# Optimization experiments

Hardware: AMD Instinct MI355X
Metric: run time of the kernel (lower is better)

Reference implementation:

```python
import jax, jax.numpy as jnp
import numpy as np


def _box_iou(a, b):
    # a: [K,4], b: [K,4] in ltrb; returns [K,K] pairwise IoU (torchvision box_iou math)
    area_a = jnp.clip(a[:, 2] - a[:, 0], 0) * jnp.clip(a[:, 3] - a[:, 1], 0)
    area_b = jnp.clip(b[:, 2] - b[:, 0], 0) * jnp.clip(b[:, 3] - b[:, 1], 0)
    lt = jnp.maximum(a[:, None, :2], b[None, :, :2])
    rb = jnp.minimum(a[:, None, 2:], b[None, :, 2:])
    wh = jnp.clip(rb - lt, 0)
    inter = wh[..., 0] * wh[..., 1]
    return inter / (area_a[:, None] + area_b[None, :] - inter + 1e-9)


def _nms_class(score, boxes, th_c, nms_th, K):
    # score: [N], boxes: [N,4]. Keep boxes with score > th_c, take top-K by score,
    # then greedy NMS suppressing lower-scored boxes with IoU >= nms_th (original keeps iou < nms_th).
    masked = jnp.where(score > th_c, score, -jnp.inf)
    top_s, idx = jax.lax.top_k(masked, K)          # descending score order
    valid = top_s > -jnp.inf
    bk = boxes[idx]                                 # [K,4]
    iou = _box_iou(bk, bk)                          # [K,K]
    order = jnp.arange(K)

    def body(alive, i):
        keep_i = alive[i]
        suppress = keep_i & (iou[i] >= nms_th) & (order > i)
        return alive & ~suppress, keep_i

    _, keep = jax.lax.scan(body, valid, order)
    return jnp.where(keep[:, None], bk, 0.0), jnp.where(keep, top_s, 0.0), keep


def decode(bboxes_in, scores_in, dboxes_xywh, conf_th, nms_th, max_num, scale_xy, scale_wh):
    B, C = bboxes_in.shape[0], scores_in.shape[1]
    K = int(max_num)
    # scale_back_batch: xywh offsets -> ltrb absolute boxes, softmax over classes
    b = jnp.transpose(bboxes_in, (0, 2, 1))                         # [B,N,4]
    xy = scale_xy * b[..., :2] * dboxes_xywh[..., 2:] + dboxes_xywh[..., :2]
    wh = jnp.exp(scale_wh * b[..., 2:]) * dboxes_xywh[..., 2:]
    ltrb = jnp.concatenate([xy - 0.5 * wh, xy + 0.5 * wh], axis=-1)  # [B,N,4]
    probs = jax.nn.softmax(jnp.transpose(scores_in, (0, 2, 1)), axis=-1)  # [B,N,C]
    cls_scores = jnp.transpose(probs[..., 1:], (0, 2, 1))            # [B,C-1,N] (skip background cls 0)

    def per_image(scores_cn, boxes_n4):
        f = jax.vmap(lambda s, t: _nms_class(s, boxes_n4, t, nms_th, K))
        return f(scores_cn, conf_th)

    bk, sk, keep = jax.vmap(per_image)(cls_scores, ltrb)  # [B,C-1,K,4], [B,C-1,K], [B,C-1,K]
    M = (C - 1) * K
    labels = jnp.arange(1, C, dtype=jnp.float32)[None, :, None] * keep.astype(jnp.float32)
    return (bk.reshape(B, M, 4), labels.reshape(B, M), sk.reshape(B, M), keep.reshape(B, M))


def setup_inputs() -> dict:
    key = jax.random.key(0)
    k0, k1, k2, k3, k4 = jax.random.split(key, 5)
    B, N, C = 32, 24564, 21
    bboxes_in = 0.5 * jax.random.normal(k0, (B, 4, N), jnp.float32)
    scores_in = jax.random.normal(k1, (B, C, N), jnp.float32)
    cxy = jax.random.uniform(k2, (1, N, 2), jnp.float32)
    dwh = jax.random.uniform(k3, (1, N, 2), jnp.float32, 0.05, 0.5)
    dboxes_xywh = jnp.concatenate([cxy, dwh], axis=-1)
    conf_th = jax.random.uniform(k4, (C - 1,), jnp.float32, 0.01, 0.05)
    return {
        'bboxes_in': bboxes_in,
        'scores_in': scores_in,
        'dboxes_xywh': dboxes_xywh,
        'conf_th': conf_th,
        'nms_th': jnp.float32(0.5),
        'max_num': 200,
        'scale_xy': 0.1,
        'scale_wh': 0.2,
    }


def reference(bboxes_in, scores_in, dboxes_xywh, conf_th, nms_th, max_num, scale_xy, scale_wh):
    # Padded, jit-compatible equivalent of the torch Decoder: per image we return
    # [(C-1)*K] slots of (boxes, labels, scores) with a boolean keep-mask; the torch
    # version returns only the kept (variable-length) entries, in the same order.
    return decode(bboxes_in, scores_in, dboxes_xywh, conf_th, nms_th, max_num, scale_xy, scale_wh)
```

## Files before the change

kernel.cpp:

```cpp
#include <hip/hip_runtime.h>
#include <math.h>

typedef unsigned int uint;
typedef unsigned short u16;
typedef unsigned long long u64;

#define NT 256
#define KTOP 200
#define CAP 256
#define CAPC 3072
#define SEGS 4
#define SEGCAP 512
#define NCLS 21
#define C1 20
#define MROWS 208
#define NSPLIT 48

struct Rec { float4 box; double lse; double pad; };

__device__ __forceinline__ u64 flip64(double d) {
  u64 u = (u64)__double_as_longlong(d);
  return (u & 0x8000000000000000ULL) ? ~u : (u | 0x8000000000000000ULL);
}

__device__ __forceinline__ double unflip64(u64 k) {
  u64 u = (k & 0x8000000000000000ULL) ? (k ^ 0x8000000000000000ULL) : ~k;
  return __longlong_as_double((long long)u);
}

__device__ __forceinline__ uint q_key16(float sf) {
  float qf = (sf + 16.0f) * 4096.0f;
  qf = fmaxf(fminf(qf, 65535.0f), 1.0f);
  return (uint)qf;
}

__device__ __forceinline__ void par_walk(const uint* hist, uint* scan, u64* wm,
                                         uint* res, uint rank, int tid) {
  scan[tid] = hist[tid];
  __syncthreads();
#pragma unroll
  for (int off = 1; off < 256; off <<= 1) {
    uint v = scan[tid];
    uint a = (tid + off < 256) ? scan[tid + off] : 0u;
    __syncthreads();
    scan[tid] = v + a;
    __syncthreads();
  }
  u64 m = __ballot(scan[tid] >= rank);
  if ((tid & 63) == 0) wm[tid >> 6] = m;
  __syncthreads();
  if (tid == 0) {
    int bin = 0;
    for (int w = 3; w >= 0; --w) {
      if (wm[w]) { bin = w * 64 + (63 - __clzll(wm[w])); break; }
    }
    res[0] = (uint)bin;
    res[1] = scan[bin];
    res[2] = hist[bin];
  }
  __syncthreads();
}

__global__ __launch_bounds__(NT) void zero_ghist(uint* __restrict__ g) {
  g[(size_t)blockIdx.x * NT + threadIdx.x] = 0;
}

__global__ __launch_bounds__(NT) void prep_kernel(
    const float* __restrict__ bboxes, const float* __restrict__ scores,
    const float* __restrict__ dboxes, const float* __restrict__ conf_th,
    const float* __restrict__ scale_xy_p, const float* __restrict__ scale_wh_p,
    Rec* __restrict__ recs, u16* __restrict__ keys_out,
    uint* __restrict__ ghist,
    int B, int N, int npad, int perblk)
{
  __shared__ double s_logth[C1];
  __shared__ uint lhist[C1 * 256];
  int tid = threadIdx.x;
  if (tid < C1) s_logth[tid] = log((double)conf_th[tid]);
  for (int i = tid; i < C1 * 256; i += NT) lhist[i] = 0;
  __syncthreads();

  int b = blockIdx.x / NSPLIT, j = blockIdx.x - b * NSPLIT;
  int s0 = j * perblk, e0 = min(N, s0 + perblk);
  int half = (e0 - s0) >> 1;
  float sxy = *scale_xy_p, swh = *scale_wh_p;

  for (int p = tid; p < half; p += NT) {
    int n = s0 + 2 * p;
    const float* bb = bboxes + (size_t)b * 4 * N + n;
    float2 bx = *reinterpret_cast<const float2*>(bb);
    float2 by = *reinterpret_cast<const float2*>(bb + (size_t)N);
    float2 bw = *reinterpret_cast<const float2*>(bb + 2 * (size_t)N);
    float2 bh = *reinterpret_cast<const float2*>(bb + 3 * (size_t)N);
    float4 d0 = reinterpret_cast<const float4*>(dboxes)[n];
    float4 d1 = reinterpret_cast<const float4*>(dboxes)[n + 1];
    float x0 = sxy * bx.x * d0.z + d0.x;
    float y0 = sxy * by.x * d0.w + d0.y;
    float w0 = expf(swh * bw.x) * d0.z;
    float h0 = expf(swh * bh.x) * d0.w;
    float x1 = sxy * bx.y * d1.z + d1.x;
    float y1 = sxy * by.y * d1.w + d1.y;
    float w1 = expf(swh * bw.y) * d1.z;
    float h1 = expf(swh * bh.y) * d1.w;

    const float* sc = scores + (size_t)b * NCLS * N + n;
    float2 v[NCLS];
    float mx0 = -INFINITY, mx1 = -INFINITY;
#pragma unroll
    for (int c = 0; c < NCLS; ++c) {
      float2 t = *reinterpret_cast<const float2*>(sc + (size_t)c * N);
      v[c] = t;
      mx0 = fmaxf(mx0, t.x);
      mx1 = fmaxf(mx1, t.y);
    }
    double a0 = 0.0, a1 = 0.0, a2 = 0.0;
    double b0 = 0.0, b1 = 0.0, b2 = 0.0;
#pragma unroll
    for (int c = 0; c < NCLS; ++c) {
      float e0f = __expf(v[c].x - mx0);
      float e1f = __expf(v[c].y - mx1);
      if ((c % 3) == 0)      { a0 += (double)e0f; b0 += (double)e1f; }
      else if ((c % 3) == 1) { a1 += (double)e0f; b1 += (double)e1f; }
      else                   { a2 += (double)e0f; b2 += (double)e1f; }
    }
    double lse0 = (double)mx0 + log(a0 + a1 + a2);
    double lse1 = (double)mx1 + log(b0 + b1 + b2);

    int gid = b * N + n;
    Rec r0, r1;
    r0.box = make_float4(x0 - 0.5f * w0, y0 - 0.5f * h0, x0 + 0.5f * w0, y0 + 0.5f * h0);
    r0.lse = lse0; r0.pad = 0.0;
    r1.box = make_float4(x1 - 0.5f * w1, y1 - 0.5f * h1, x1 + 0.5f * w1, y1 + 0.5f * h1);
    r1.lse = lse1; r1.pad = 0.0;
    recs[gid] = r0;
    recs[gid + 1] = r1;

#pragma unroll
    for (int c = 0; c < C1; ++c) {
      double s0d = (double)v[c + 1].x - lse0;
      double s1d = (double)v[c + 1].y - lse1;
      uint k0 = 0, k1 = 0;
      if (s0d > s_logth[c]) k0 = q_key16((float)s0d);
      if (s1d > s_logth[c]) k1 = q_key16((float)s1d);
      *reinterpret_cast<uint*>(keys_out + ((size_t)b * C1 + c) * npad + n)
          = k0 | (k1 << 16);
      if (k0) atomicAdd(&lhist[c * 256 + (k0 >> 8)], 1u);
      if (k1) atomicAdd(&lhist[c * 256 + (k1 >> 8)], 1u);
    }
  }
  if (j == NSPLIT - 1 && npad > N) {
    int pad = npad - N;
    for (int t = tid; t < pad * C1; t += NT) {
      int c = t / pad, n = N + (t - c * pad);
      keys_out[((size_t)b * C1 + c) * npad + n] = 0;
    }
  }
  __syncthreads();
  for (int i = tid; i < C1 * 256; i += NT) {
    uint v2 = lhist[i];
    if (v2) atomicAdd(&ghist[((size_t)b * C1 + (i >> 8)) * 256 + (i & 255)], v2);
  }
}

__global__ __launch_bounds__(NT) void collect_kernel(
    const u16* __restrict__ keys, const uint* __restrict__ ghist,
    uint4* __restrict__ L0cnt, uint* __restrict__ cand, uint* __restrict__ cnts,
    int npad)
{
  int blk = blockIdx.x;
  int task = blk >> 2, seg = blk & (SEGS - 1);
  int tid = threadIdx.x, lane = tid & 63;
  __shared__ uint sL, sCnt0, sCnt;

  if (tid < 64) {
    uint4 h = reinterpret_cast<const uint4*>(ghist + (size_t)task * 256)[tid];
    uint s = h.x + h.y + h.z + h.w;
    uint suf = s;
#pragma unroll
    for (int off = 1; off < 64; off <<= 1) {
      uint o = (uint)__shfl_down((int)suf, off);
      if (lane + off < 64) suf += o;
    }
    uint total = (uint)__shfl((int)suf, 0);
    uint sn = (uint)__shfl_down((int)suf, 1);
    if (lane == 63) sn = 0;
    uint c3 = h.w + sn, c2 = c3 + h.z, c1 = c2 + h.y, c0 = c1 + h.x;
    uint binoff, cnt, abv;
    if (c3 >= KTOP)      { binoff = 3; cnt = c3; abv = c3 - h.w; }
    else if (c2 >= KTOP) { binoff = 2; cnt = c2; abv = c2 - h.z; }
    else if (c1 >= KTOP) { binoff = 1; cnt = c1; abv = c1 - h.y; }
    else                 { binoff = 0; cnt = c0; abv = c0 - h.x; }
    uint L0v, cnt0v, abovev;
    if (total < KTOP) {
      L0v = 1u; cnt0v = total; abovev = 0u;
    } else {
      u64 m = __ballot(suf >= KTOP);
      int l = 63 - __clzll(m);
      uint bo = (uint)__shfl((int)binoff, l);
      cnt0v = (uint)__shfl((int)cnt, l);
      abovev = (uint)__shfl((int)abv, l);
      L0v = ((uint)(4 * l) + bo) << 8;
    }
    if (lane == 0) {
      sL = L0v; sCnt0 = cnt0v;
      if (seg == 0) L0cnt[task] = make_uint4(L0v, cnt0v, abovev, total);
    }
  }
  if (tid == NT - 1) sCnt = 0;
  __syncthreads();

  uint L = sL, cnt0 = sCnt0;
  if (cnt0 > CAPC) { if (tid == 0) cnts[blk] = 0; return; }

  const u16* krow = keys + (size_t)task * npad;
  const uint4* krow8 = reinterpret_cast<const uint4*>(krow);
  int nv8 = npad >> 3;
  int per8 = (nv8 + SEGS - 1) >> 2;
  int s8 = seg * per8, e8 = min(nv8, s8 + per8);
  uint* myc = cand + ((size_t)task * SEGS + seg) * SEGCAP;

  for (int i = s8 + tid; i < e8; i += NT) {
    uint4 kv = krow8[i];
    uint base = (uint)(i << 3);
    uint ks[8] = { kv.x & 0xFFFFu, kv.x >> 16, kv.y & 0xFFFFu, kv.y >> 16,
                   kv.z & 0xFFFFu, kv.z >> 16, kv.w & 0xFFFFu, kv.w >> 16 };
#pragma unroll
    for (int comp = 0; comp < 8; ++comp) {
      uint k = ks[comp];
      bool f = (k >= L);
      u64 m = __ballot(f);
      if (m) {
        uint nb = (uint)__popcll(m);
        uint wb = 0;
        if (lane == 0) wb = atomicAdd(&sCnt, nb);
        wb = (uint)__shfl((int)wb, 0);
        if (f) {
          uint pos = wb + (uint)__popcll(m & ((1ULL << lane) - 1ULL));
          if (pos < SEGCAP) myc[pos] = (k << 15) | (base + comp);
        }
      }
    }
  }
  __syncthreads();
  if (tid == 0) cnts[blk] = sCnt;
}

__global__ __launch_bounds__(NT) void final_kernel(
    const u16* __restrict__ keys, const uint4* __restrict__ L0cnt,
    const uint* __restrict__ candg, const uint* __restrict__ cnts,
    const float* __restrict__ scores, const Rec* __restrict__ recs,
    const float* __restrict__ nms_th_p,
    float* __restrict__ out, int B, int N, int npad)
{
  int task = blockIdx.x;
  int b = task / C1, c = task - b * C1;
  int tid = threadIdx.x, lane = tid & 63, wav = tid >> 6;
  const u16* krow = keys + (size_t)task * npad;
  int nv8 = npad >> 3;

  __shared__ uint cand[CAPC];
  __shared__ uint histB[256];
  __shared__ uint scanB[256];
  __shared__ u64 wmB[4];
  __shared__ uint res3[4];
  __shared__ uint scq[SEGS];
  __shared__ int si[CAP];
  __shared__ u64 sC[CAP];
  __shared__ u64 skid[CAP];
  __shared__ float4 sbx[CAP];
  __shared__ float4 sbox[MROWS];
  __shared__ float sar[MROWS];
  __shared__ u64 smaskT[13][64];
  __shared__ u64 saliveW[4];
  __shared__ uint sCnt, sCnt2;

  uint4 w0 = L0cnt[task];
  uint cnt0 = w0.y;
  if (tid < SEGS) scq[tid] = cnts[task * SEGS + tid];
  if (tid == 0) { sCnt = 0; sCnt2 = 0; }
  if (tid < MROWS) { sbox[tid] = make_float4(0.f, 0.f, 0.f, 0.f); sar[tid] = 0.f; }
  __syncthreads();
  bool slow = (cnt0 > CAPC) ||
              (scq[0] > SEGCAP) || (scq[1] > SEGCAP) ||
              (scq[2] > SEGCAP) || (scq[3] > SEGCAP);

  uint pref = w0.x >> 8, above = w0.z, rank = KTOP - w0.z;
  uint cnt;

  if (!slow) {
    uint off1 = scq[0], off2 = off1 + scq[1], off3 = off2 + scq[2];
    cnt = off3 + scq[3];
    const uint* cg = candg + (size_t)task * SEGS * SEGCAP;
    for (int j = tid; j < (int)scq[0]; j += NT) cand[j] = cg[j];
    for (int j = tid; j < (int)scq[1]; j += NT) cand[off1 + j] = cg[SEGCAP + j];
    for (int j = tid; j < (int)scq[2]; j += NT) cand[off2 + j] = cg[2 * SEGCAP + j];
    for (int j = tid; j < (int)scq[3]; j += NT) cand[off3 + j] = cg[3 * SEGCAP + j];
    __syncthreads();
  } else {
    const uint4* krow8 = reinterpret_cast<const uint4*>(krow);
    histB[tid] = 0;
    __syncthreads();
    for (int i = tid; i < nv8; i += NT) {
      uint4 kv = krow8[i];
      uint ks[8] = { kv.x & 0xFFFFu, kv.x >> 16, kv.y & 0xFFFFu, kv.y >> 16,
                     kv.z & 0xFFFFu, kv.z >> 16, kv.w & 0xFFFFu, kv.w >> 16 };
#pragma unroll
      for (int comp = 0; comp < 8; ++comp) {
        uint k = ks[comp];
        if ((k >> 8) == pref) atomicAdd(&histB[k & 255u], 1u);
      }
    }
    __syncthreads();
    par_walk(histB, scanB, wmB, res3, rank, tid);
    uint Ts = (pref << 8) | res3[0];
    for (int i = tid; i < nv8; i += NT) {
      uint4 kv = krow8[i];
      uint base = (uint)(i << 3);
      uint ks[8] = { kv.x & 0xFFFFu, kv.x >> 16, kv.y & 0xFFFFu, kv.y >> 16,
                     kv.z & 0xFFFFu, kv.z >> 16, kv.w & 0xFFFFu, kv.w >> 16 };
#pragma unroll
      for (int comp = 0; comp < 8; ++comp) {
        uint k = ks[comp];
        bool f = (k >= Ts);
        u64 m = __ballot(f);
        if (m) {
          uint nb = (uint)__popcll(m);
          uint wb = 0;
          if (lane == 0) wb = atomicAdd(&sCnt, nb);
          wb = (uint)__shfl((int)wb, 0);
          if (f) {
            uint pos = wb + (uint)__popcll(m & ((1ULL << lane) - 1ULL));
            if (pos < CAPC) cand[pos] = (k << 15) | (base + comp);
          }
        }
      }
    }
    __syncthreads();
    cnt = min(sCnt, (uint)CAPC);
  }

  uint cntF;
  if (cnt <= CAP) {
    for (int p = tid; p < (int)cnt; p += NT) si[p] = (int)(cand[p] & 0x7FFFu);
    __syncthreads();
    cntF = cnt;
  } else {
    histB[tid] = 0;
    __syncthreads();
    for (int p = tid; p < (int)cnt; p += NT) {
      uint k = cand[p] >> 15;
      if ((k >> 8) == pref) atomicAdd(&histB[k & 255u], 1u);
    }
    __syncthreads();
    par_walk(histB, scanB, wmB, res3, rank, tid);
    uint T = (pref << 8) | res3[0];
    for (int p = tid; p < (int)cnt; p += NT) {
      uint cd = cand[p];
      if ((cd >> 15) >= T) {
        uint q = atomicAdd(&sCnt2, 1u);
        if (q < CAP) si[q] = (int)(cd & 0x7FFFu);
      }
    }
    __syncthreads();
    cntF = min(sCnt2, (uint)CAP);
  }

  int valid_cnt = (int)min(cntF, (uint)KTOP);

  {
    int p = tid;
    u64 C;
    if (p < (int)cntF) {
      int n = si[p];
      const Rec* rc = recs + (size_t)b * N + n;
      float4 box = rc->box;
      double l = rc->lse;
      double s = (double)scores[((size_t)b * NCLS + (c + 1)) * N + n] - l;
      u64 f = flip64(s);
      C = (f & ~0x7FFFULL) | (u64)(32767 - n);
      sbx[p] = box;
    } else {
      C = (u64)p;
      sbx[p] = make_float4(0.f, 0.f, 0.f, 0.f);
    }
    sC[p] = C;
  }
  __syncthreads();

  {
    u64 kp = sC[tid];
    int r = 0;
#pragma unroll 8
    for (int jj = 0; jj < CAP; ++jj) r += (sC[jj] > kp) ? 1 : 0;
    if (tid < (int)cntF && r < KTOP) {
      skid[r] = kp;
      float4 bx = sbx[tid];
      sbox[r] = bx;
      sar[r] = fmaxf(bx.z - bx.x, 0.f) * fmaxf(bx.w - bx.y, 0.f);
    }
  }
  __syncthreads();

  float nth = *nms_th_p;

  {
    float4 jb0 = sbox[lane], jb1 = sbox[lane + 64], jb2 = sbox[lane + 128];
    float4 jb3 = (lane + 192 < MROWS) ? sbox[lane + 192]
                                      : make_float4(0.f, 0.f, 0.f, 0.f);
    float ja0 = sar[lane], ja1 = sar[lane + 64], ja2 = sar[lane + 128],
          ja3 = (lane + 192 < MROWS) ? sar[lane + 192] : 0.f;
    for (int w = wav; w < 13; w += 4) {
      u64 word = 0;
      int r0 = w * 16;
#pragma unroll
      for (int rr = 0; rr < 16; ++rr) {
        int r = r0 + rr;
        float4 rb = sbox[r];
        float ra = sar[r];
        uint nib = 0;
#define IOU_BIT(K, JB, JA) { \
        int j = lane + 64 * (K); \
        float xx1 = fmaxf(rb.x, JB.x), yy1 = fmaxf(rb.y, JB.y); \
        float xx2 = fminf(rb.z, JB.z), yy2 = fminf(rb.w, JB.w); \
        float ww = fmaxf(xx2 - xx1, 0.f), hh = fmaxf(yy2 - yy1, 0.f); \
        float inter = ww * hh; \
        float den = ((ra + JA) - inter) + 1e-9f; \
        if ((inter >= nth * den) && (j > r)) nib |= 1u << (K); }
        IOU_BIT(0, jb0, ja0) IOU_BIT(1, jb1, ja1)
        IOU_BIT(2, jb2, ja2) IOU_BIT(3, jb3, ja3)
#undef IOU_BIT
        word |= (u64)nib << (rr * 4);
      }
      smaskT[w][lane] = word;
    }
  }
  __syncthreads();

  if (tid < 64) {
    u64 mm[13];
#pragma unroll
    for (int w = 0; w < 13; ++w) mm[w] = smaskT[w][lane];
    uint av = 0;
#pragma unroll
    for (int k = 0; k < 4; ++k)
      if (lane + 64 * k < valid_cnt) av |= 1u << k;
#define STEP(i) { \
    u64 bm = __ballot((lane == ((i) & 63)) && ((av >> ((i) >> 6)) & 1u)); \
    if (bm) av &= ~((uint)((mm[(i) >> 4] >> (((i) & 15) * 4)) & 0xFULL)); }
#define S4(i)  STEP(i) STEP((i)+1) STEP((i)+2) STEP((i)+3)
#define S16(i) S4(i) S4((i)+4) S4((i)+8) S4((i)+12)
#define S64(i) S16(i) S16((i)+16) S16((i)+32) S16((i)+48)
    S64(0) S64(64) S64(128) S16(192)
#undef S64
#undef S16
#undef S4
#undef STEP
#pragma unroll
    for (int k = 0; k < 4; ++k) {
      u64 bb2 = __ballot((av >> k) & 1u);
      if (lane == 0) saliveW[k] = bb2;
    }
  }
  __syncthreads();

  size_t M = (size_t)C1 * KTOP;
  float* out_boxes  = out;
  float* out_labels = out + (size_t)B * M * 4;
  float* out_scores = out_labels + (size_t)B * M;
  float* out_keep   = out_scores + (size_t)B * M;
  if (tid < KTOP) {
    size_t slot = ((size_t)b * C1 + c) * KTOP + tid;
    bool kept = (tid < valid_cnt) && ((saliveW[tid >> 6] >> (tid & 63)) & 1ULL);
    float4 bx = kept ? sbox[tid] : make_float4(0.f, 0.f, 0.f, 0.f);
    reinterpret_cast<float4*>(out_boxes)[slot] = bx;
    out_labels[slot] = kept ? (float)(c + 1) : 0.0f;
    out_scores[slot] = kept ? (float)exp(unflip64(skid[tid])) : 0.0f;
    out_keep[slot]   = kept ? 1.0f : 0.0f;
  }
}

extern "C" void kernel_launch(void* const* d_in, const int* in_sizes, int n_in,
                              void* d_out, int out_size, void* d_ws, size_t ws_size,
                              hipStream_t stream) {
  const float* bboxes   = (const float*)d_in[0];
  const float* scores   = (const float*)d_in[1];
  const float* dboxes   = (const float*)d_in[2];
  const float* conf_th  = (const float*)d_in[3];
  const float* nms_th   = (const float*)d_in[4];
  const float* scale_xy = (const float*)d_in[6];
  const float* scale_wh = (const float*)d_in[7];

  int N = in_sizes[2] / 4;
  int B = in_sizes[0] / (4 * N);
  int npad = (N + 7) & ~7;

  char* ws = (char*)d_ws;
  size_t off = 0;
  Rec*    recs    = (Rec*)   (ws + off); off += (size_t)B * N * sizeof(Rec);
  u16*    keys    = (u16*)   (ws + off); off += (size_t)B * C1 * npad * 2;
  uint*   ghist   = (uint*)  (ws + off); off += (size_t)B * C1 * 256 * 4;
  uint4*  L0cnt   = (uint4*) (ws + off); off += (size_t)B * C1 * 16;
  uint*   cand    = (uint*)  (ws + off); off += (size_t)B * C1 * SEGS * SEGCAP * 4;
  uint*   cnts    = (uint*)  (ws + off);

  zero_ghist<<<B * C1, NT, 0, stream>>>(ghist);

  int perblk = ((N + NSPLIT - 1) / NSPLIT + 1) & ~1;
  prep_kernel<<<B * NSPLIT, NT, 0, stream>>>(
      bboxes, scores, dboxes, conf_th, scale_xy, scale_wh,
      recs, keys, ghist, B, N, npad, perblk);

  collect_kernel<<<B * C1 * SEGS, NT, 0, stream>>>(
      keys, ghist, L0cnt, cand, cnts, npad);

  final_kernel<<<B * C1, NT, 0, stream>>>(
      keys, L0cnt, cand, cnts, scores, recs, nms_th,
      (float*)d_out, B, N, npad);
}
```

Before: 92.44 us.

## Split final kernel into top-k selection and NMS mask/resolve kernels

The final per-(image,class) kernel is divided into a top-k kernel, which writes the sorted top-200 keys and boxes to workspace, and a separate NMS kernel that builds the IoU bitmask and resolves survivors. Each kernel now needs less shared memory, so more blocks can be resident per CU. The cost is an extra launch and a global-memory round trip for the top-k keys and boxes.

```diff
diff --git a/kernel.cpp b/kernel.cpp
--- a/kernel.cpp
+++ b/kernel.cpp
@@ -245,16 +245,16 @@
   if (tid == 0) cnts[blk] = sCnt;
 }
 
-__global__ __launch_bounds__(NT) void final_kernel(
+__global__ __launch_bounds__(NT) void topk_kernel(
     const u16* __restrict__ keys, const uint4* __restrict__ L0cnt,
     const uint* __restrict__ candg, const uint* __restrict__ cnts,
     const float* __restrict__ scores, const Rec* __restrict__ recs,
-    const float* __restrict__ nms_th_p,
-    float* __restrict__ out, int B, int N, int npad)
+    u64* __restrict__ tkeys, float4* __restrict__ tbox, uint* __restrict__ tcnt,
+    int B, int N, int npad)
 {
   int task = blockIdx.x;
   int b = task / C1, c = task - b * C1;
-  int tid = threadIdx.x, lane = tid & 63, wav = tid >> 6;
+  int tid = threadIdx.x, lane = tid & 63;
   const u16* krow = keys + (size_t)task * npad;
   int nv8 = npad >> 3;
 
@@ -266,19 +266,13 @@
   __shared__ uint scq[SEGS];
   __shared__ int si[CAP];
   __shared__ u64 sC[CAP];
-  __shared__ u64 skid[CAP];
   __shared__ float4 sbx[CAP];
-  __shared__ float4 sbox[MROWS];
-  __shared__ float sar[MROWS];
-  __shared__ u64 smaskT[13][64];
-  __shared__ u64 saliveW[4];
   __shared__ uint sCnt, sCnt2;
 
   uint4 w0 = L0cnt[task];
   uint cnt0 = w0.y;
   if (tid < SEGS) scq[tid] = cnts[task * SEGS + tid];
   if (tid == 0) { sCnt = 0; sCnt2 = 0; }
-  if (tid < MROWS) { sbox[tid] = make_float4(0.f, 0.f, 0.f, 0.f); sar[tid] = 0.f; }
   __syncthreads();
   bool slow = (cnt0 > CAPC) ||
               (scq[0] > SEGCAP) || (scq[1] > SEGCAP) ||
@@ -365,8 +359,6 @@
     cntF = min(sCnt2, (uint)CAP);
   }
 
-  int valid_cnt = (int)min(cntF, (uint)KTOP);
-
   {
     int p = tid;
     u64 C;
@@ -392,16 +384,38 @@
     int r = 0;
 #pragma unroll 8
     for (int jj = 0; jj < CAP; ++jj) r += (sC[jj] > kp) ? 1 : 0;
-    if (tid < (int)cntF && r < KTOP) {
-      skid[r] = kp;
-      float4 bx = sbx[tid];
-      sbox[r] = bx;
-      sar[r] = fmaxf(bx.z - bx.x, 0.f) * fmaxf(bx.w - bx.y, 0.f);
-    }
-  }
-  __syncthreads();
-
+    if (r < KTOP) {
+      tkeys[(size_t)task * KTOP + r] = kp;
+      tbox[(size_t)task * KTOP + r] = sbx[tid];
+    }
+  }
+  if (tid == 0) tcnt[task] = min(cntF, (uint)KTOP);
+}
+
+__global__ __launch_bounds__(NT) void maskresolve_kernel(
+    const u64* __restrict__ tkeys, const float4* __restrict__ tbox,
+    const uint* __restrict__ tcnt, const float* __restrict__ nms_th_p,
+    float* __restrict__ out, int B)
+{
+  int task = blockIdx.x;
+  int b = task / C1, c = task - b * C1;
+  int tid = threadIdx.x, lane = tid & 63, wav = tid >> 6;
+
+  __shared__ float4 sbox[MROWS];
+  __shared__ float sar[MROWS];
+  __shared__ u64 smaskT[13][64];
+  __shared__ u64 saliveW[4];
+
+  int valid = (int)tcnt[task];
   float nth = *nms_th_p;
+
+  if (tid < MROWS) {
+    float4 bx = (tid < valid) ? tbox[(size_t)task * KTOP + tid]
+                              : make_float4(0.f, 0.f, 0.f, 0.f);
+    sbox[tid] = bx;
+    sar[tid] = fmaxf(bx.z - bx.x, 0.f) * fmaxf(bx.w - bx.y, 0.f);
+  }
+  __syncthreads();
 
   {
     float4 jb0 = sbox[lane], jb1 = sbox[lane + 64], jb2 = sbox[lane + 128];
@@ -443,7 +457,7 @@
     uint av = 0;
 #pragma unroll
     for (int k = 0; k < 4; ++k)
-      if (lane + 64 * k < valid_cnt) av |= 1u << k;
+      if (lane + 64 * k < valid) av |= 1u << k;
 #define STEP(i) { \
     u64 bm = __ballot((lane == ((i) & 63)) && ((av >> ((i) >> 6)) & 1u)); \
     if (bm) av &= ~((uint)((mm[(i) >> 4] >> (((i) & 15) * 4)) & 0xFULL)); }
@@ -470,11 +484,11 @@
   float* out_keep   = out_scores + (size_t)B * M;
   if (tid < KTOP) {
     size_t slot = ((size_t)b * C1 + c) * KTOP + tid;
-    bool kept = (tid < valid_cnt) && ((saliveW[tid >> 6] >> (tid & 63)) & 1ULL);
+    bool kept = (tid < valid) && ((saliveW[tid >> 6] >> (tid & 63)) & 1ULL);
     float4 bx = kept ? sbox[tid] : make_float4(0.f, 0.f, 0.f, 0.f);
     reinterpret_cast<float4*>(out_boxes)[slot] = bx;
     out_labels[slot] = kept ? (float)(c + 1) : 0.0f;
-    out_scores[slot] = kept ? (float)exp(unflip64(skid[tid])) : 0.0f;
+    out_scores[slot] = kept ? (float)exp(unflip64(tkeys[(size_t)task * KTOP + tid])) : 0.0f;
     out_keep[slot]   = kept ? 1.0f : 0.0f;
   }
 }
@@ -501,7 +515,10 @@
   uint*   ghist   = (uint*)  (ws + off); off += (size_t)B * C1 * 256 * 4;
   uint4*  L0cnt   = (uint4*) (ws + off); off += (size_t)B * C1 * 16;
   uint*   cand    = (uint*)  (ws + off); off += (size_t)B * C1 * SEGS * SEGCAP * 4;
-  uint*   cnts    = (uint*)  (ws + off);
+  uint*   cnts    = (uint*)  (ws + off); off += (size_t)B * C1 * SEGS * 4;
+  u64*    tkeys   = (u64*)   (ws + off); off += (size_t)B * C1 * KTOP * 8;
+  float4* tbox    = (float4*)(ws + off); off += (size_t)B * C1 * KTOP * 16;
+  uint*   tcnt    = (uint*)  (ws + off);
 
   zero_ghist<<<B * C1, NT, 0, stream>>>(ghist);
 
@@ -513,7 +530,9 @@
   collect_kernel<<<B * C1 * SEGS, NT, 0, stream>>>(
       keys, ghist, L0cnt, cand, cnts, npad);
 
-  final_kernel<<<B * C1, NT, 0, stream>>>(
-      keys, L0cnt, cand, cnts, scores, recs, nms_th,
-      (float*)d_out, B, N, npad);
-}
+  topk_kernel<<<B * C1, NT, 0, stream>>>(
+      keys, L0cnt, cand, cnts, scores, recs, tkeys, tbox, tcnt, B, N, npad);
+
+  maskresolve_kernel<<<B * C1, NT, 0, stream>>>(
+      tkeys, tbox, tcnt, nms_th, (float*)d_out, B);
+}
```

New measurement: 95.78 us. +3.6%, slower.
